# Kernel tuning notes

Measured on AMD Instinct MI355X. Metric: run time of the kernel, lower is better.

## Reference

```python
import jax, jax.numpy as jnp
import numpy as np

T, B = 128, 256
C_IN, H = 1024, 1024


def setup_inputs() -> dict:
    key = jax.random.key(0)
    ks = jax.random.split(key, 6)
    x = jax.random.normal(ks[0], (T * B, C_IN), dtype=jnp.float32)
    Wi = jax.random.normal(ks[1], (C_IN, 4 * H), dtype=jnp.float32) / np.sqrt(C_IN)
    Wh = jax.random.normal(ks[2], (H, 4 * H), dtype=jnp.float32) / np.sqrt(H)
    b = jax.random.normal(ks[3], (4 * H,), dtype=jnp.float32) * 0.01
    done = jax.random.randint(ks[4], (T * B,), 0, 2) > 0
    main = jax.random.randint(ks[5], (T * B,), 0, 2) > 0
    zeros = jnp.zeros((B, H), dtype=jnp.float32)
    return {"x": x, "c1": zeros, "h1": zeros, "c2": zeros, "h2": zeros,
            "Wi": Wi, "Wh": Wh, "b": b, "done": done, "main": main}


def reference(x, c1, h1, c2, h2, Wi, Wh, b, done, main):
    batch = c1.shape[0]
    num_steps = x.shape[0] // batch
    x3 = x.reshape(num_steps, batch, -1)
    done3 = done.reshape(num_steps, batch)
    main3 = main.reshape(num_steps, batch)

    def step(carry, inp):
        (r1c, r1h), (r2c, r2h) = carry
        xt, dt, mt = inp
        m = mt[:, None]  # [B,1] select player-1 vs player-2 state
        c = jnp.where(m, r1c, r2c)
        h = jnp.where(m, r1h, r2h)
        # OptimizedLSTMCell: fused gates, flax order i, f, g, o
        z = xt @ Wi + h @ Wh + b
        i, f, g, o = jnp.split(z, 4, axis=-1)
        nc = jax.nn.sigmoid(f) * c + jax.nn.sigmoid(i) * jnp.tanh(g)
        nh = jax.nn.sigmoid(o) * jnp.tanh(nc)
        # write back only to the active player's state
        n1c = jnp.where(m, nc, r1c); n1h = jnp.where(m, nh, r1h)
        n2c = jnp.where(m, r2c, nc); n2h = jnp.where(m, r2h, nh)
        # reset both states where episode is done
        d = dt[:, None]
        n1c = jnp.where(d, 0.0, n1c); n1h = jnp.where(d, 0.0, n1h)
        n2c = jnp.where(d, 0.0, n2c); n2h = jnp.where(d, 0.0, n2h)
        return ((n1c, n1h), (n2c, n2h)), nh

    _, ys = jax.lax.scan(step, ((c1, h1), (c2, h2)), (x3, done3, main3))
    return ys.reshape(-1, ys.shape[-1])  # [T*B, H]
```

## Files before the change

kernel.cpp:

```cpp
#include <hip/hip_runtime.h>
#include <cstdint>
#include <cstddef>

typedef unsigned short u16;
typedef unsigned char u8;
typedef unsigned int u32;

typedef short s16x8 __attribute__((ext_vector_type(8)));
typedef float f32x4 __attribute__((ext_vector_type(4)));

__device__ __forceinline__ float b2f(u16 h){ u32 u = ((u32)h)<<16; float f; __builtin_memcpy(&f,&u,4); return f; }
__device__ __forceinline__ u16 f2b(float x){ u32 u; __builtin_memcpy(&u,&x,4); u += 0x7fffu + ((u>>16)&1u); return (u16)(u>>16); }
__device__ __forceinline__ float sigf(float x){ return 1.f/(1.f+__expf(-x)); }
__device__ __forceinline__ float tanh2(float x){
  float ax=fabsf(x); float e=__expf(-2.f*ax); float r=(1.f-e)/(1.f+e); return x<0.f? -r : r;
}

typedef __attribute__((address_space(1))) const void gvoid_t;
typedef __attribute__((address_space(3))) void lvoid_t;
__device__ __forceinline__ void gl_lds16(const u16* src, u16* dst){
  __builtin_amdgcn_global_load_lds((gvoid_t*)src, (lvoid_t*)dst, 16, 0, 0);
}

__device__ __forceinline__ void st_u16_coh(u16* p, u16 v){
  asm volatile("global_store_short %0, %1, off sc0 sc1" :: "v"(p), "v"((u32)v) : "memory");
}
__device__ __forceinline__ void st_f32_coh(float* p, float v){
  asm volatile("global_store_dword %0, %1, off sc0 sc1" :: "v"(p), "v"(v) : "memory");
}
__device__ __forceinline__ s16x8 gload16(const u16* p){
  s16x8 r;
  asm volatile("global_load_dwordx4 %0, %1, off" : "=v"(r) : "v"(p) : "memory");
  return r;
}
__device__ __forceinline__ s16x8 gload16_coh(const u16* p){
  s16x8 r;
  asm volatile("global_load_dwordx4 %0, %1, off sc0 sc1" : "=v"(r) : "v"(p) : "memory");
  return r;
}

__global__ void detect_mask_mode(const u8* raw, int n, int* flag){
  __shared__ int cnt;
  int tid = threadIdx.x;
  if(tid==0) cnt=0;
  __syncthreads();
  int c=0;
  for(int i=tid;i<n;i+=blockDim.x) c += (raw[i]!=0);
  atomicAdd(&cnt, c);
  __syncthreads();
  if(tid==0) *flag = (cnt > (n>>2)) ? 1 : 0;
}

__global__ void convert_masks(const void* done_raw, const void* main_raw, u8* done_u8, u8* main_u8, int n, const int* flag){
  int mode = *flag;
  for(int i = blockIdx.x*blockDim.x + threadIdx.x; i<n; i += gridDim.x*blockDim.x){
    u8 d, m;
    if(mode){ d = ((const u8*)done_raw)[i]!=0; m = ((const u8*)main_raw)[i]!=0; }
    else    { d = ((const int*)done_raw)[i]!=0; m = ((const int*)main_raw)[i]!=0; }
    done_u8[i]=d; main_u8[i]=m;
  }
}

__global__ void zero_flags(int* p, int n){
  int i = threadIdx.x;
  if(i<n) p[i]=0;
}

__global__ void cvt_f32_bf16(const float* __restrict__ in, u16* __restrict__ out, int n4){
  int i = blockIdx.x*blockDim.x + threadIdx.x;
  if(i < n4){
    float4 v = ((const float4*)in)[i];
    ushort4 o;
    o.x=f2b(v.x); o.y=f2b(v.y); o.z=f2b(v.z); o.w=f2b(v.w);
    ((ushort4*)out)[i]=o;
  }
}

__global__ void transpose_to_bf16(const float* __restrict__ in, u16* __restrict__ out, int R, int C){
  __shared__ float tile[64][65];
  int c0 = blockIdx.x*64, r0 = blockIdx.y*64;
  int tx = threadIdx.x & 63, ty = threadIdx.x >> 6;
  for(int i=ty;i<64;i+=4) tile[i][tx] = in[(size_t)(r0+i)*C + c0 + tx];
  __syncthreads();
  for(int i=ty;i<64;i+=4) out[(size_t)(c0+i)*R + r0 + tx] = f2b(tile[tx][i]);
}

__global__ void init_hsel(const float* __restrict__ h1in, const float* __restrict__ h2in,
                          const u8* __restrict__ mmain, u16* __restrict__ hsel0){
  int i = blockIdx.x*blockDim.x + threadIdx.x;
  if(i < 256*1024){
    int row = i >> 10;
    hsel0[i] = f2b(mmain[row] ? h1in[i] : h2in[i]);
  }
}

template<bool ZF32>
__global__ __launch_bounds__(256) void gemm_zx(const u16* __restrict__ A, const u16* __restrict__ Bt,
                                               const float* __restrict__ bias, void* __restrict__ Cout,
                                               int M, int N, int K){
  __shared__ u16 As[128*32];
  __shared__ u16 Bs[128*32];
  int nbx = N>>7, nby = M>>7;
  int nwg = nbx*nby;
  int gid = blockIdx.x;
  int per = nwg>>3;
  int g2 = (gid&7)*per + (gid>>3);
  int tpg = 8*nbx;
  int grp = g2/tpg, w = g2%tpg;
  int brow = grp*8 + (w & 7);
  int bcol = w >> 3;
  int row0 = brow<<7, col0 = bcol<<7;

  int tid=threadIdx.x, wid=tid>>6, lane=tid&63;
  int l15=lane&15, hi=lane>>4;
  int wm=(wid>>1)<<6, wn=(wid&1)<<6;

  f32x4 acc[4][4];
  #pragma unroll
  for(int m=0;m<4;m++)
    #pragma unroll
    for(int n=0;n<4;n++) acc[m][n]=(f32x4){0.f,0.f,0.f,0.f};

  for(int k0=0;k0<K;k0+=32){
    __syncthreads();
    #pragma unroll
    for(int q=0;q<2;q++){
      int cb=q*256+wid*64;
      int ch=cb+lane;
      gl_lds16(A + (size_t)(row0+(ch>>2))*K + k0 + (ch&3)*8, &As[cb*8]);
    }
    #pragma unroll
    for(int q=0;q<2;q++){
      int cb=q*256+wid*64;
      int ch=cb+lane;
      gl_lds16(Bt + (size_t)(col0+(ch>>2))*K + k0 + (ch&3)*8, &Bs[cb*8]);
    }
    __syncthreads();
    s16x8 a[4], b[4];
    #pragma unroll
    for(int m=0;m<4;m++) a[m] = *(const s16x8*)&As[(wm+m*16+l15)*32 + hi*8];
    #pragma unroll
    for(int n=0;n<4;n++) b[n] = *(const s16x8*)&Bs[(wn+n*16+l15)*32 + hi*8];
    #pragma unroll
    for(int m=0;m<4;m++)
      #pragma unroll
      for(int n=0;n<4;n++)
        acc[m][n] = __builtin_amdgcn_mfma_f32_16x16x32_bf16(a[m],b[n],acc[m][n],0,0,0);
  }
  #pragma unroll
  for(int m=0;m<4;m++){
    #pragma unroll
    for(int n=0;n<4;n++){
      #pragma unroll
      for(int j=0;j<4;j++){
        int r = row0+wm+m*16+hi*4+j;
        int c = col0+wn+n*16+l15;
        float v = acc[m][n][j] + bias[c];
        if(ZF32) ((float*)Cout)[(size_t)r*N+c]=v;
        else     ((u16*)Cout)[(size_t)r*N+c]=f2b(v);
      }
    }
  }
}

template<bool ZF32>
__global__ __launch_bounds__(512) __attribute__((amdgpu_waves_per_eu(2,2)))
void lstm_persist(
    const void* __restrict__ Zx, const u16* __restrict__ Wht,
    u16* __restrict__ hs0, u16* __restrict__ hs1,
    const float* __restrict__ c1i, const float* __restrict__ h1i,
    const float* __restrict__ c2i, const float* __restrict__ h2i,
    const u8* __restrict__ mdone, const u8* __restrict__ mmain,
    float* __restrict__ out, int* __restrict__ ready)
{
  __shared__ u16 As[32768];
  __shared__ float zpart[4*2*32*33];

  const int bid = blockIdx.x;
  const int rg = bid & 7, jg = bid >> 3;
  const int r0 = rg << 5, j0 = jg << 5;
  const int tid = threadIdx.x, wid = tid >> 6, lane = tid & 63;
  const int l15 = lane & 15, hi = lane >> 4;
  const int gate = wid >> 1, kg = wid & 1;
  const int srow = tid >> 4, sc16 = tid & 15;
  const int erow = tid >> 5, ecol = tid & 31;

  s16x8 breg[2][16];
  {
    #pragma unroll
    for(int n=0;n<2;n++){
      const u16* wp = Wht + ((size_t)(gate*1024 + j0 + n*16 + l15))*1024 + kg*512 + hi*8;
      #pragma unroll
      for(int kk=0;kk<16;kk++) breg[n][kk] = gload16(wp + kk*32);
    }
    asm volatile("s_waitcnt vmcnt(0)" ::: "memory");
    __builtin_amdgcn_sched_barrier(0);
  }

  float c1r[2],c2r[2],h1r[2],h2r[2];
  #pragma unroll
  for(int e=0;e<2;e++){
    size_t sidx = (size_t)(r0 + e*16 + erow)*1024 + j0 + ecol;
    c1r[e]=c1i[sidx]; c2r[e]=c2i[sidx]; h1r[e]=h1i[sidx]; h2r[e]=h2i[sidx];
  }

  const u16* Zb = (const u16*)Zx;
  const float* Zf = (const float*)Zx;
  int* flag = ready + rg*32;

  for(int t=0;t<128;t++){
    float zr[4][2]; u8 md[2], mm[2], mm2[2];
    #pragma unroll
    for(int e=0;e<2;e++){
      int gb = t*256 + r0 + e*16 + erow;
      size_t base = (size_t)gb*4096 + j0 + ecol;
      #pragma unroll
      for(int g=0; g<4; g++)
        zr[g][e] = ZF32 ? Zf[base + g*1024] : b2f(Zb[base + g*1024]);
      md[e]=mdone[gb]; mm[e]=mmain[gb];
      mm2[e] = (t<127) ? mmain[gb+256] : (u8)0;
    }

    if(t>0 && tid==0){
      while(__hip_atomic_load(flag, __ATOMIC_RELAXED, __HIP_MEMORY_SCOPE_AGENT) < 32*t)
        __builtin_amdgcn_s_sleep(1);
    }
    __syncthreads();
    __builtin_amdgcn_sched_barrier(0);

    const u16* hin = (t&1) ? hs1 : hs0;
    u16* hout = (t&1) ? hs0 : hs1;

    {
      const u16* hrow = hin + (size_t)(r0+srow)*1024;
      s16x8 v[8];
      #pragma unroll
      for(int kc=0;kc<8;kc++) v[kc] = gload16_coh(hrow + (kc*16+sc16)*8);
      asm volatile("s_waitcnt vmcnt(4)" ::: "memory");
      #pragma unroll
      for(int kc=0;kc<4;kc++){
        int chunk = kc*16+sc16;
        *(s16x8*)&As[chunk*256 + ((srow ^ (chunk&7))<<3)] = v[kc];
      }
      asm volatile("s_waitcnt vmcnt(0)" ::: "memory");
      #pragma unroll
      for(int kc=4;kc<8;kc++){
        int chunk = kc*16+sc16;
        *(s16x8*)&As[chunk*256 + ((srow ^ (chunk&7))<<3)] = v[kc];
      }
    }
    __syncthreads();

    f32x4 acc[2][2];
    #pragma unroll
    for(int m=0;m<2;m++)
      #pragma unroll
      for(int n=0;n<2;n++) acc[m][n]=(f32x4){0.f,0.f,0.f,0.f};
    #pragma unroll
    for(int kk=0;kk<16;kk++){
      int c0 = (kg*16 + kk)*4 + hi;
      s16x8 a0 = *(const s16x8*)&As[c0*256 + ((l15      ^ (c0&7))<<3)];
      s16x8 a1 = *(const s16x8*)&As[c0*256 + (((16+l15) ^ (c0&7))<<3)];
      acc[0][0] = __builtin_amdgcn_mfma_f32_16x16x32_bf16(a0, breg[0][kk], acc[0][0], 0,0,0);
      acc[0][1] = __builtin_amdgcn_mfma_f32_16x16x32_bf16(a0, breg[1][kk], acc[0][1], 0,0,0);
      acc[1][0] = __builtin_amdgcn_mfma_f32_16x16x32_bf16(a1, breg[0][kk], acc[1][0], 0,0,0);
      acc[1][1] = __builtin_amdgcn_mfma_f32_16x16x32_bf16(a1, breg[1][kk], acc[1][1], 0,0,0);
    }

    #pragma unroll
    for(int m=0;m<2;m++)
      #pragma unroll
      for(int n=0;n<2;n++)
        #pragma unroll
        for(int j=0;j<4;j++){
          int row = m*16 + hi*4 + j;
          zpart[((gate*2+kg)*32 + row)*33 + n*16 + l15] = acc[m][n][j];
        }
    __syncthreads();

    float nhv[2];
    #pragma unroll
    for(int e=0;e<2;e++){
      int row = e*16 + erow;
      float zi  = zr[0][e] + zpart[((0)*32+row)*33 + ecol] + zpart[((1)*32+row)*33 + ecol];
      float zf_ = zr[1][e] + zpart[((2)*32+row)*33 + ecol] + zpart[((3)*32+row)*33 + ecol];
      float zg  = zr[2][e] + zpart[((4)*32+row)*33 + ecol] + zpart[((5)*32+row)*33 + ecol];
      float zo  = zr[3][e] + zpart[((6)*32+row)*33 + ecol] + zpart[((7)*32+row)*33 + ecol];
      bool m_ = mm[e]!=0, d_ = md[e]!=0;
      float co = m_ ? c1r[e] : c2r[e];
      float nc = sigf(zf_)*co + sigf(zi)*tanh2(zg);
      float nhx = sigf(zo)*tanh2(nc);
      nhv[e] = nhx;
      float n1c = m_?nc:c1r[e], n2c = m_?c2r[e]:nc;
      float n1h = m_?nhx:h1r[e], n2h = m_?h2r[e]:nhx;
      if(d_){ n1c=0.f; n2c=0.f; n1h=0.f; n2h=0.f; }
      c1r[e]=n1c; c2r[e]=n2c; h1r[e]=n1h; h2r[e]=n2h;
      if(t<127)
        st_u16_coh(&hout[(size_t)(r0+row)*1024 + j0 + ecol], f2b(mm2[e] ? n1h : n2h));
    }
    asm volatile("s_waitcnt vmcnt(0)" ::: "memory");
    __syncthreads();
    if(t<127 && tid==0)
      __hip_atomic_fetch_add(flag, 1, __ATOMIC_RELAXED, __HIP_MEMORY_SCOPE_AGENT);

    #pragma unroll
    for(int e=0;e<2;e++){
      int gb = t*256 + r0 + e*16 + erow;
      st_f32_coh(&out[(size_t)gb*1024 + j0 + ecol], nhv[e]);
    }
  }
}

extern "C" void kernel_launch(void* const* d_in, const int* in_sizes, int n_in,
                              void* d_out, int out_size, void* d_ws, size_t ws_size,
                              hipStream_t stream){
  const float* x   = (const float*)d_in[0];
  const float* c1i = (const float*)d_in[1];
  const float* h1i = (const float*)d_in[2];
  const float* c2i = (const float*)d_in[3];
  const float* h2i = (const float*)d_in[4];
  const float* Wi  = (const float*)d_in[5];
  const float* Wh  = (const float*)d_in[6];
  const float* bias= (const float*)d_in[7];
  const void* done_raw = d_in[8];
  const void* main_raw = d_in[9];
  float* out = (float*)d_out;

  char* ws = (char*)d_ws;
  size_t off=0;
  auto alloc=[&](size_t sz)->char*{ char* p = ws+off; off += (sz+255)&~(size_t)255; return p; };

  u16* xb   = (u16*)alloc(33554432ull*2);
  u16* WiT  = (u16*)alloc(4096ull*1024*2);
  u16* WhT  = (u16*)alloc(4096ull*1024*2);
  u16* hs0  = (u16*)alloc(262144ull*2);
  u16* hs1  = (u16*)alloc(262144ull*2);
  u8* dmask = (u8*)alloc(32768);
  u8* mmask = (u8*)alloc(32768);
  int* flag = (int*)alloc(256);
  int* ready= (int*)alloc(1024);

  bool zf32 = (off + 536870912ull) <= ws_size;
  void* Zx  = (void*)alloc(zf32 ? 536870912ull : 268435456ull);

  detect_mask_mode<<<1,256,0,stream>>>((const u8*)done_raw, 32768, flag);
  convert_masks<<<64,256,0,stream>>>(done_raw, main_raw, dmask, mmask, 32768, flag);
  cvt_f32_bf16<<<32768,256,0,stream>>>(x, xb, 8388608);
  transpose_to_bf16<<<dim3(64,16),256,0,stream>>>(Wi, WiT, 1024, 4096);
  transpose_to_bf16<<<dim3(64,16),256,0,stream>>>(Wh, WhT, 1024, 4096);
  init_hsel<<<1024,256,0,stream>>>(h1i, h2i, mmask, hs0);
  zero_flags<<<1,256,0,stream>>>(ready, 256);

  if(zf32) gemm_zx<true ><<<8192,256,0,stream>>>(xb, WiT, bias, Zx, 32768, 4096, 1024);
  else     gemm_zx<false><<<8192,256,0,stream>>>(xb, WiT, bias, Zx, 32768, 4096, 1024);

  if(zf32)
    lstm_persist<true ><<<256,512,0,stream>>>(Zx,WhT,hs0,hs1,c1i,h1i,c2i,h2i,dmask,mmask,out,ready);
  else
    lstm_persist<false><<<256,512,0,stream>>>(Zx,WhT,hs0,hs1,c1i,h1i,c2i,h2i,dmask,mmask,out,ready);
}
```

Before: 1.103 ms.

## Streamline persistent LSTM step: packed masks, SGPR-based addressing, per-wave signal counting

Packs the done, main and next-step main masks into a single byte code. The persistent LSTM loop now uses precomputed 32-bit voffsets with scalar base pointers for its loads and stores, and uses fast reciprocal in sigmoid and tanh. The block-wide barrier before the cross-block ready signal is replaced by an LDS counter, so the eighth wave to finish issues the global atomic increment. This removes a __syncthreads and some address arithmetic from the recurrent critical path. In exchange, LDS counter reuse across steps depends on careful ordering, and rcp slightly reduces precision.

```diff
diff --git a/kernel.cpp b/kernel.cpp
--- a/kernel.cpp
+++ b/kernel.cpp
@@ -11,9 +11,11 @@
 
 __device__ __forceinline__ float b2f(u16 h){ u32 u = ((u32)h)<<16; float f; __builtin_memcpy(&f,&u,4); return f; }
 __device__ __forceinline__ u16 f2b(float x){ u32 u; __builtin_memcpy(&u,&x,4); u += 0x7fffu + ((u>>16)&1u); return (u16)(u>>16); }
-__device__ __forceinline__ float sigf(float x){ return 1.f/(1.f+__expf(-x)); }
+__device__ __forceinline__ float sigf(float x){ return __builtin_amdgcn_rcpf(1.f+__expf(-x)); }
 __device__ __forceinline__ float tanh2(float x){
-  float ax=fabsf(x); float e=__expf(-2.f*ax); float r=(1.f-e)/(1.f+e); return x<0.f? -r : r;
+  float ax=fabsf(x); float e=__expf(-2.f*ax);
+  float r=(1.f-e)*__builtin_amdgcn_rcpf(1.f+e);
+  return x<0.f? -r : r;
 }
 
 typedef __attribute__((address_space(1))) const void gvoid_t;
@@ -22,20 +24,25 @@
   __builtin_amdgcn_global_load_lds((gvoid_t*)src, (lvoid_t*)dst, 16, 0, 0);
 }
 
-__device__ __forceinline__ void st_u16_coh(u16* p, u16 v){
-  asm volatile("global_store_short %0, %1, off sc0 sc1" :: "v"(p), "v"((u32)v) : "memory");
-}
-__device__ __forceinline__ void st_f32_coh(float* p, float v){
-  asm volatile("global_store_dword %0, %1, off sc0 sc1" :: "v"(p), "v"(v) : "memory");
+__device__ __forceinline__ s16x8 gload16_coh_s(const u16* sbase, u32 voff){
+  s16x8 r;
+  asm volatile("global_load_dwordx4 %0, %1, %2 sc0 sc1" : "=v"(r) : "v"(voff), "s"(sbase) : "memory");
+  return r;
+}
+__device__ __forceinline__ float gloadf_s(const float* sbase, u32 voff){
+  float r;
+  asm volatile("global_load_dword %0, %1, %2" : "=v"(r) : "v"(voff), "s"(sbase) : "memory");
+  return r;
+}
+__device__ __forceinline__ void st_u16_coh_s(u16* sbase, u32 voff, u16 v){
+  asm volatile("global_store_short %0, %1, %2 sc0 sc1" :: "v"(voff), "v"((u32)v), "s"(sbase) : "memory");
+}
+__device__ __forceinline__ void st_f32_coh_s(float* sbase, u32 voff, float v){
+  asm volatile("global_store_dword %0, %1, %2 sc0 sc1" :: "v"(voff), "v"(v), "s"(sbase) : "memory");
 }
 __device__ __forceinline__ s16x8 gload16(const u16* p){
   s16x8 r;
   asm volatile("global_load_dwordx4 %0, %1, off" : "=v"(r) : "v"(p) : "memory");
-  return r;
-}
-__device__ __forceinline__ s16x8 gload16_coh(const u16* p){
-  s16x8 r;
-  asm volatile("global_load_dwordx4 %0, %1, off sc0 sc1" : "=v"(r) : "v"(p) : "memory");
   return r;
 }
 
@@ -51,13 +58,18 @@
   if(tid==0) *flag = (cnt > (n>>2)) ? 1 : 0;
 }
 
-__global__ void convert_masks(const void* done_raw, const void* main_raw, u8* done_u8, u8* main_u8, int n, const int* flag){
+__global__ void build_mcode(const void* done_raw, const void* main_raw, u8* code, int n, const int* flag){
   int mode = *flag;
   for(int i = blockIdx.x*blockDim.x + threadIdx.x; i<n; i += gridDim.x*blockDim.x){
-    u8 d, m;
-    if(mode){ d = ((const u8*)done_raw)[i]!=0; m = ((const u8*)main_raw)[i]!=0; }
-    else    { d = ((const int*)done_raw)[i]!=0; m = ((const int*)main_raw)[i]!=0; }
-    done_u8[i]=d; main_u8[i]=m;
+    u8 d, m, m2;
+    if(mode){
+      d = ((const u8*)done_raw)[i]!=0; m = ((const u8*)main_raw)[i]!=0;
+      m2 = (i+256<n) ? (((const u8*)main_raw)[i+256]!=0) : (u8)0;
+    } else {
+      d = ((const int*)done_raw)[i]!=0; m = ((const int*)main_raw)[i]!=0;
+      m2 = (i+256<n) ? (((const int*)main_raw)[i+256]!=0) : (u8)0;
+    }
+    code[i] = d | (m<<1) | (m2<<2);
   }
 }
 
@@ -86,11 +98,11 @@
 }
 
 __global__ void init_hsel(const float* __restrict__ h1in, const float* __restrict__ h2in,
-                          const u8* __restrict__ mmain, u16* __restrict__ hsel0){
+                          const u8* __restrict__ mcode, u16* __restrict__ hsel0){
   int i = blockIdx.x*blockDim.x + threadIdx.x;
   if(i < 256*1024){
     int row = i >> 10;
-    hsel0[i] = f2b(mmain[row] ? h1in[i] : h2in[i]);
+    hsel0[i] = f2b((mcode[row]&2) ? h1in[i] : h2in[i]);
   }
 }
 
@@ -170,11 +182,12 @@
     u16* __restrict__ hs0, u16* __restrict__ hs1,
     const float* __restrict__ c1i, const float* __restrict__ h1i,
     const float* __restrict__ c2i, const float* __restrict__ h2i,
-    const u8* __restrict__ mdone, const u8* __restrict__ mmain,
+    const u8* __restrict__ mcode,
     float* __restrict__ out, int* __restrict__ ready)
 {
   __shared__ u16 As[32768];
   __shared__ float zpart[4*2*32*33];
+  __shared__ int lcnt[2];
 
   const int bid = blockIdx.x;
   const int rg = bid & 7, jg = bid >> 3;
@@ -185,6 +198,8 @@
   const int srow = tid >> 4, sc16 = tid & 15;
   const int erow = tid >> 5, ecol = tid & 31;
 
+  if(tid < 2) lcnt[tid] = 0;
+
   s16x8 breg[2][16];
   {
     #pragma unroll
@@ -204,22 +219,52 @@
     c1r[e]=c1i[sidx]; c2r[e]=c2i[sidx]; h1r[e]=h1i[sidx]; h2r[e]=h2i[sidx];
   }
 
-  const u16* Zb = (const u16*)Zx;
-  const float* Zf = (const float*)Zx;
+  u32 voffS[8];
+  #pragma unroll
+  for(int kc=0;kc<8;kc++) voffS[kc] = (u32)(((r0+srow)*1024 + (kc*16+sc16)*8)*2);
+  u32 voffH[2], voffO[2];
+  #pragma unroll
+  for(int e=0;e<2;e++){
+    u32 idx = (u32)((r0 + e*16 + erow)*1024 + j0 + ecol);
+    voffH[e] = idx*2;
+    voffO[e] = idx*4;
+  }
+  u32 voffZ[8];
+  #pragma unroll
+  for(int g=0;g<4;g++)
+    #pragma unroll
+    for(int e=0;e<2;e++)
+      voffZ[g*2+e] = (u32)((((r0 + e*16 + erow)*4096) + g*1024 + j0 + ecol)*4);
+
+  u16* pS = &As[sc16*256 + ((srow ^ (sc16&7))<<3)];
+  const u16* pAe = &As[kg*16384 + hi*256 + ((l15 ^  hi   )<<3)];
+  const u16* pAo = &As[kg*16384 + hi*256 + ((l15 ^ (4+hi))<<3)];
+  float* pzw = &zpart[((gate*2+kg)*32 + hi*4)*33 + l15];
+  const float* pzr = &zpart[erow*33 + ecol];
+
+  const char* zstep = (const char*)Zx;
+  const u16* Zb16 = (const u16*)Zx;
+  float* outp = out;
+  const u8* mp = mcode + r0;
   int* flag = ready + rg*32;
 
+  #pragma unroll 1
   for(int t=0;t<128;t++){
-    float zr[4][2]; u8 md[2], mm[2], mm2[2];
-    #pragma unroll
-    for(int e=0;e<2;e++){
-      int gb = t*256 + r0 + e*16 + erow;
-      size_t base = (size_t)gb*4096 + j0 + ecol;
-      #pragma unroll
-      for(int g=0; g<4; g++)
-        zr[g][e] = ZF32 ? Zf[base + g*1024] : b2f(Zb[base + g*1024]);
-      md[e]=mdone[gb]; mm[e]=mmain[gb];
-      mm2[e] = (t<127) ? mmain[gb+256] : (u8)0;
-    }
+    float zr[4][2];
+    if(ZF32){
+      #pragma unroll
+      for(int g=0;g<4;g++)
+        #pragma unroll
+        for(int e=0;e<2;e++)
+          zr[g][e] = gloadf_s((const float*)zstep, voffZ[g*2+e]);
+    } else {
+      #pragma unroll
+      for(int g=0;g<4;g++)
+        #pragma unroll
+        for(int e=0;e<2;e++)
+          zr[g][e] = b2f(Zb16[(size_t)(t*256 + r0 + e*16 + erow)*4096 + g*1024 + j0 + ecol]);
+    }
+    u8 cd0 = mp[erow], cd1 = mp[16+erow];
 
     if(t>0 && tid==0){
       while(__hip_atomic_load(flag, __ATOMIC_RELAXED, __HIP_MEMORY_SCOPE_AGENT) < 32*t)
@@ -228,26 +273,16 @@
     __syncthreads();
     __builtin_amdgcn_sched_barrier(0);
 
-    const u16* hin = (t&1) ? hs1 : hs0;
-    u16* hout = (t&1) ? hs0 : hs1;
+    const u16* hinp = (t&1) ? hs1 : hs0;
+    u16* houtp = (t&1) ? hs0 : hs1;
 
     {
-      const u16* hrow = hin + (size_t)(r0+srow)*1024;
-      s16x8 v[8];
-      #pragma unroll
-      for(int kc=0;kc<8;kc++) v[kc] = gload16_coh(hrow + (kc*16+sc16)*8);
-      asm volatile("s_waitcnt vmcnt(4)" ::: "memory");
-      #pragma unroll
-      for(int kc=0;kc<4;kc++){
-        int chunk = kc*16+sc16;
-        *(s16x8*)&As[chunk*256 + ((srow ^ (chunk&7))<<3)] = v[kc];
-      }
+      s16x8 hv[8];
+      #pragma unroll
+      for(int kc=0;kc<8;kc++) hv[kc] = gload16_coh_s(hinp, voffS[kc]);
       asm volatile("s_waitcnt vmcnt(0)" ::: "memory");
       #pragma unroll
-      for(int kc=4;kc<8;kc++){
-        int chunk = kc*16+sc16;
-        *(s16x8*)&As[chunk*256 + ((srow ^ (chunk&7))<<3)] = v[kc];
-      }
+      for(int kc=0;kc<8;kc++) *(s16x8*)(pS + kc*4096) = hv[kc];
     }
     __syncthreads();
 
@@ -258,9 +293,9 @@
       for(int n=0;n<2;n++) acc[m][n]=(f32x4){0.f,0.f,0.f,0.f};
     #pragma unroll
     for(int kk=0;kk<16;kk++){
-      int c0 = (kg*16 + kk)*4 + hi;
-      s16x8 a0 = *(const s16x8*)&As[c0*256 + ((l15      ^ (c0&7))<<3)];
-      s16x8 a1 = *(const s16x8*)&As[c0*256 + (((16+l15) ^ (c0&7))<<3)];
+      const u16* p = (kk&1) ? pAo : pAe;
+      s16x8 a0 = *(const s16x8*)(p + kk*1024);
+      s16x8 a1 = *(const s16x8*)(p + kk*1024 + 128);
       acc[0][0] = __builtin_amdgcn_mfma_f32_16x16x32_bf16(a0, breg[0][kk], acc[0][0], 0,0,0);
       acc[0][1] = __builtin_amdgcn_mfma_f32_16x16x32_bf16(a0, breg[1][kk], acc[0][1], 0,0,0);
       acc[1][0] = __builtin_amdgcn_mfma_f32_16x16x32_bf16(a1, breg[0][kk], acc[1][0], 0,0,0);
@@ -272,21 +307,19 @@
       #pragma unroll
       for(int n=0;n<2;n++)
         #pragma unroll
-        for(int j=0;j<4;j++){
-          int row = m*16 + hi*4 + j;
-          zpart[((gate*2+kg)*32 + row)*33 + n*16 + l15] = acc[m][n][j];
-        }
+        for(int j=0;j<4;j++)
+          pzw[m*528 + j*33 + n*16] = acc[m][n][j];
     __syncthreads();
 
     float nhv[2];
     #pragma unroll
     for(int e=0;e<2;e++){
-      int row = e*16 + erow;
-      float zi  = zr[0][e] + zpart[((0)*32+row)*33 + ecol] + zpart[((1)*32+row)*33 + ecol];
-      float zf_ = zr[1][e] + zpart[((2)*32+row)*33 + ecol] + zpart[((3)*32+row)*33 + ecol];
-      float zg  = zr[2][e] + zpart[((4)*32+row)*33 + ecol] + zpart[((5)*32+row)*33 + ecol];
-      float zo  = zr[3][e] + zpart[((6)*32+row)*33 + ecol] + zpart[((7)*32+row)*33 + ecol];
-      bool m_ = mm[e]!=0, d_ = md[e]!=0;
+      u8 cd = e ? cd1 : cd0;
+      float zi  = zr[0][e] + pzr[0*1056 + e*528] + pzr[1*1056 + e*528];
+      float zf_ = zr[1][e] + pzr[2*1056 + e*528] + pzr[3*1056 + e*528];
+      float zg  = zr[2][e] + pzr[4*1056 + e*528] + pzr[5*1056 + e*528];
+      float zo  = zr[3][e] + pzr[6*1056 + e*528] + pzr[7*1056 + e*528];
+      bool d_ = cd & 1, m_ = cd & 2, m2 = cd & 4;
       float co = m_ ? c1r[e] : c2r[e];
       float nc = sigf(zf_)*co + sigf(zi)*tanh2(zg);
       float nhx = sigf(zo)*tanh2(nc);
@@ -296,18 +329,27 @@
       if(d_){ n1c=0.f; n2c=0.f; n1h=0.f; n2h=0.f; }
       c1r[e]=n1c; c2r[e]=n2c; h1r[e]=n1h; h2r[e]=n2h;
       if(t<127)
-        st_u16_coh(&hout[(size_t)(r0+row)*1024 + j0 + ecol], f2b(mm2[e] ? n1h : n2h));
-    }
-    asm volatile("s_waitcnt vmcnt(0)" ::: "memory");
-    __syncthreads();
-    if(t<127 && tid==0)
-      __hip_atomic_fetch_add(flag, 1, __ATOMIC_RELAXED, __HIP_MEMORY_SCOPE_AGENT);
-
-    #pragma unroll
-    for(int e=0;e<2;e++){
-      int gb = t*256 + r0 + e*16 + erow;
-      st_f32_coh(&out[(size_t)gb*1024 + j0 + ecol], nhv[e]);
-    }
+        st_u16_coh_s(houtp, voffH[e], f2b(m2 ? n1h : n2h));
+    }
+
+    if(t<127){
+      asm volatile("s_waitcnt vmcnt(0)" ::: "memory");
+      if(lane==0){
+        int c = atomicAdd(&lcnt[t&1], 1);
+        if(c==7){
+          lcnt[t&1] = 0;
+          __hip_atomic_fetch_add(flag, 1, __ATOMIC_RELAXED, __HIP_MEMORY_SCOPE_AGENT);
+        }
+      }
+    }
+
+    #pragma unroll
+    for(int e=0;e<2;e++)
+      st_f32_coh_s(outp, voffO[e], nhv[e]);
+
+    zstep += 4194304;
+    outp  += 262144;
+    mp    += 256;
   }
 }
 
@@ -335,8 +377,7 @@
   u16* WhT  = (u16*)alloc(4096ull*1024*2);
   u16* hs0  = (u16*)alloc(262144ull*2);
   u16* hs1  = (u16*)alloc(262144ull*2);
-  u8* dmask = (u8*)alloc(32768);
-  u8* mmask = (u8*)alloc(32768);
+  u8* mcode = (u8*)alloc(32768);
   int* flag = (int*)alloc(256);
   int* ready= (int*)alloc(1024);
 
@@ -344,18 +385,18 @@
   void* Zx  = (void*)alloc(zf32 ? 536870912ull : 268435456ull);
 
   detect_mask_mode<<<1,256,0,stream>>>((const u8*)done_raw, 32768, flag);
-  convert_masks<<<64,256,0,stream>>>(done_raw, main_raw, dmask, mmask, 32768, flag);
+  build_mcode<<<64,256,0,stream>>>(done_raw, main_raw, mcode, 32768, flag);
   cvt_f32_bf16<<<32768,256,0,stream>>>(x, xb, 8388608);
   transpose_to_bf16<<<dim3(64,16),256,0,stream>>>(Wi, WiT, 1024, 4096);
   transpose_to_bf16<<<dim3(64,16),256,0,stream>>>(Wh, WhT, 1024, 4096);
-  init_hsel<<<1024,256,0,stream>>>(h1i, h2i, mmask, hs0);
+  init_hsel<<<1024,256,0,stream>>>(h1i, h2i, mcode, hs0);
   zero_flags<<<1,256,0,stream>>>(ready, 256);
 
   if(zf32) gemm_zx<true ><<<8192,256,0,stream>>>(xb, WiT, bias, Zx, 32768, 4096, 1024);
   else     gemm_zx<false><<<8192,256,0,stream>>>(xb, WiT, bias, Zx, 32768, 4096, 1024);
 
   if(zf32)
-    lstm_persist<true ><<<256,512,0,stream>>>(Zx,WhT,hs0,hs1,c1i,h1i,c2i,h2i,dmask,mmask,out,ready);
+    lstm_persist<true ><<<256,512,0,stream>>>(Zx,WhT,hs0,hs1,c1i,h1i,c2i,h2i,mcode,out,ready);
   else
-    lstm_persist<false><<<256,512,0,stream>>>(Zx,WhT,hs0,hs1,c1i,h1i,c2i,h2i,dmask,mmask,out,ready);
-}
+    lstm_persist<false><<<256,512,0,stream>>>(Zx,WhT,hs0,hs1,c1i,h1i,c2i,h2i,mcode,out,ready);
+}
```

Result: slower. 1.289 ms (+16.9%).

## Store input projection as fp16, deepen GEMM K-tile, use fast reciprocal

Applied to the files above, without the earlier changes.

The precomputed input-projection Zx is always stored as 16-bit fp16 instead of fp32 when workspace allows, which halves the GEMM's output writes and the persistent LSTM's per-step Zx reads. The GEMM now stages 64-wide K slices in a k-chunk-major LDS layout with two MFMA sub-steps per barrier pair, and hoists the bias load out of the inner loop. Sigmoid and tanh use the hardware approximate reciprocal instead of division. fp16 storage and the approximate reciprocal cost some precision.

```diff
diff --git a/kernel.cpp b/kernel.cpp
--- a/kernel.cpp
+++ b/kernel.cpp
@@ -9,11 +9,17 @@
 typedef short s16x8 __attribute__((ext_vector_type(8)));
 typedef float f32x4 __attribute__((ext_vector_type(4)));
 
+#define MF(a,b,c) __builtin_amdgcn_mfma_f32_16x16x32_bf16((a),(b),(c),0,0,0)
+
 __device__ __forceinline__ float b2f(u16 h){ u32 u = ((u32)h)<<16; float f; __builtin_memcpy(&f,&u,4); return f; }
 __device__ __forceinline__ u16 f2b(float x){ u32 u; __builtin_memcpy(&u,&x,4); u += 0x7fffu + ((u>>16)&1u); return (u16)(u>>16); }
-__device__ __forceinline__ float sigf(float x){ return 1.f/(1.f+__expf(-x)); }
+__device__ __forceinline__ u16 f2h(float x){ _Float16 h = (_Float16)x; u16 u; __builtin_memcpy(&u,&h,2); return u; }
+__device__ __forceinline__ float h2f(u16 v){ _Float16 h; __builtin_memcpy(&h,&v,2); return (float)h; }
+__device__ __forceinline__ float sigf(float x){ return __builtin_amdgcn_rcpf(1.f+__expf(-x)); }
 __device__ __forceinline__ float tanh2(float x){
-  float ax=fabsf(x); float e=__expf(-2.f*ax); float r=(1.f-e)/(1.f+e); return x<0.f? -r : r;
+  float ax=fabsf(x); float e=__expf(-2.f*ax);
+  float r=(1.f-e)*__builtin_amdgcn_rcpf(1.f+e);
+  return x<0.f? -r : r;
 }
 
 typedef __attribute__((address_space(1))) const void gvoid_t;
@@ -94,14 +100,12 @@
   }
 }
 
-template<bool ZF32>
 __global__ __launch_bounds__(256) void gemm_zx(const u16* __restrict__ A, const u16* __restrict__ Bt,
-                                               const float* __restrict__ bias, void* __restrict__ Cout,
-                                               int M, int N, int K){
-  __shared__ u16 As[128*32];
-  __shared__ u16 Bs[128*32];
-  int nbx = N>>7, nby = M>>7;
-  int nwg = nbx*nby;
+                                               const float* __restrict__ bias, u16* __restrict__ C){
+  __shared__ u16 As[8192];
+  __shared__ u16 Bs[8192];
+  const int nbx = 32;
+  const int nwg = 8192;
   int gid = blockIdx.x;
   int per = nwg>>3;
   int g2 = (gid&7)*per + (gid>>3);
@@ -121,52 +125,55 @@
     #pragma unroll
     for(int n=0;n<4;n++) acc[m][n]=(f32x4){0.f,0.f,0.f,0.f};
 
-  for(int k0=0;k0<K;k0+=32){
-    __syncthreads();
-    #pragma unroll
-    for(int q=0;q<2;q++){
-      int cb=q*256+wid*64;
-      int ch=cb+lane;
-      gl_lds16(A + (size_t)(row0+(ch>>2))*K + k0 + (ch&3)*8, &As[cb*8]);
-    }
-    #pragma unroll
-    for(int q=0;q<2;q++){
-      int cb=q*256+wid*64;
-      int ch=cb+lane;
-      gl_lds16(Bt + (size_t)(col0+(ch>>2))*K + k0 + (ch&3)*8, &Bs[cb*8]);
-    }
-    __syncthreads();
-    s16x8 a[4], b[4];
-    #pragma unroll
-    for(int m=0;m<4;m++) a[m] = *(const s16x8*)&As[(wm+m*16+l15)*32 + hi*8];
-    #pragma unroll
-    for(int n=0;n<4;n++) b[n] = *(const s16x8*)&Bs[(wn+n*16+l15)*32 + hi*8];
-    #pragma unroll
-    for(int m=0;m<4;m++)
-      #pragma unroll
-      for(int n=0;n<4;n++)
-        acc[m][n] = __builtin_amdgcn_mfma_f32_16x16x32_bf16(a[m],b[n],acc[m][n],0,0,0);
+  for(int k0=0;k0<1024;k0+=64){
+    __syncthreads();
+    #pragma unroll
+    for(int i=0;i<4;i++){
+      int cb = (wid*4+i)*64;
+      int c  = cb + lane;
+      int r  = c & 127, s = c >> 7;
+      gl_lds16(A + (size_t)(row0+r)*1024 + k0 + s*8, &As[cb*8]);
+    }
+    #pragma unroll
+    for(int i=0;i<4;i++){
+      int cb = (wid*4+i)*64;
+      int c  = cb + lane;
+      int r  = c & 127, s = c >> 7;
+      gl_lds16(Bt + (size_t)(col0+r)*1024 + k0 + s*8, &Bs[cb*8]);
+    }
+    __syncthreads();
+    #pragma unroll
+    for(int kk=0;kk<2;kk++){
+      s16x8 a[4], b[4];
+      #pragma unroll
+      for(int m=0;m<4;m++) a[m] = *(const s16x8*)&As[(kk*4+hi)*1024 + (wm+m*16+l15)*8];
+      #pragma unroll
+      for(int n=0;n<4;n++) b[n] = *(const s16x8*)&Bs[(kk*4+hi)*1024 + (wn+n*16+l15)*8];
+      #pragma unroll
+      for(int m=0;m<4;m++)
+        #pragma unroll
+        for(int n=0;n<4;n++)
+          acc[m][n] = MF(a[m],b[n],acc[m][n]);
+    }
   }
   #pragma unroll
   for(int m=0;m<4;m++){
     #pragma unroll
     for(int n=0;n<4;n++){
+      int c = col0+wn+n*16+l15;
+      float bv = bias[c];
       #pragma unroll
       for(int j=0;j<4;j++){
         int r = row0+wm+m*16+hi*4+j;
-        int c = col0+wn+n*16+l15;
-        float v = acc[m][n][j] + bias[c];
-        if(ZF32) ((float*)Cout)[(size_t)r*N+c]=v;
-        else     ((u16*)Cout)[(size_t)r*N+c]=f2b(v);
+        C[(size_t)r*4096+c] = f2h(acc[m][n][j] + bv);
       }
     }
   }
 }
 
-template<bool ZF32>
 __global__ __launch_bounds__(512) __attribute__((amdgpu_waves_per_eu(2,2)))
 void lstm_persist(
-    const void* __restrict__ Zx, const u16* __restrict__ Wht,
+    const u16* __restrict__ Zx, const u16* __restrict__ Wht,
     u16* __restrict__ hs0, u16* __restrict__ hs1,
     const float* __restrict__ c1i, const float* __restrict__ h1i,
     const float* __restrict__ c2i, const float* __restrict__ h2i,
@@ -204,8 +211,6 @@
     c1r[e]=c1i[sidx]; c2r[e]=c2i[sidx]; h1r[e]=h1i[sidx]; h2r[e]=h2i[sidx];
   }
 
-  const u16* Zb = (const u16*)Zx;
-  const float* Zf = (const float*)Zx;
   int* flag = ready + rg*32;
 
   for(int t=0;t<128;t++){
@@ -216,7 +221,7 @@
       size_t base = (size_t)gb*4096 + j0 + ecol;
       #pragma unroll
       for(int g=0; g<4; g++)
-        zr[g][e] = ZF32 ? Zf[base + g*1024] : b2f(Zb[base + g*1024]);
+        zr[g][e] = h2f(Zx[base + g*1024]);
       md[e]=mdone[gb]; mm[e]=mmain[gb];
       mm2[e] = (t<127) ? mmain[gb+256] : (u8)0;
     }
@@ -261,10 +266,10 @@
       int c0 = (kg*16 + kk)*4 + hi;
       s16x8 a0 = *(const s16x8*)&As[c0*256 + ((l15      ^ (c0&7))<<3)];
       s16x8 a1 = *(const s16x8*)&As[c0*256 + (((16+l15) ^ (c0&7))<<3)];
-      acc[0][0] = __builtin_amdgcn_mfma_f32_16x16x32_bf16(a0, breg[0][kk], acc[0][0], 0,0,0);
-      acc[0][1] = __builtin_amdgcn_mfma_f32_16x16x32_bf16(a0, breg[1][kk], acc[0][1], 0,0,0);
-      acc[1][0] = __builtin_amdgcn_mfma_f32_16x16x32_bf16(a1, breg[0][kk], acc[1][0], 0,0,0);
-      acc[1][1] = __builtin_amdgcn_mfma_f32_16x16x32_bf16(a1, breg[1][kk], acc[1][1], 0,0,0);
+      acc[0][0] = MF(a0, breg[0][kk], acc[0][0]);
+      acc[0][1] = MF(a0, breg[1][kk], acc[0][1]);
+      acc[1][0] = MF(a1, breg[0][kk], acc[1][0]);
+      acc[1][1] = MF(a1, breg[1][kk], acc[1][1]);
     }
 
     #pragma unroll
@@ -339,9 +344,7 @@
   u8* mmask = (u8*)alloc(32768);
   int* flag = (int*)alloc(256);
   int* ready= (int*)alloc(1024);
-
-  bool zf32 = (off + 536870912ull) <= ws_size;
-  void* Zx  = (void*)alloc(zf32 ? 536870912ull : 268435456ull);
+  u16* Zx   = (u16*)alloc(268435456ull);
 
   detect_mask_mode<<<1,256,0,stream>>>((const u8*)done_raw, 32768, flag);
   convert_masks<<<64,256,0,stream>>>(done_raw, main_raw, dmask, mmask, 32768, flag);
@@ -351,11 +354,7 @@
   init_hsel<<<1024,256,0,stream>>>(h1i, h2i, mmask, hs0);
   zero_flags<<<1,256,0,stream>>>(ready, 256);
 
-  if(zf32) gemm_zx<true ><<<8192,256,0,stream>>>(xb, WiT, bias, Zx, 32768, 4096, 1024);
-  else     gemm_zx<false><<<8192,256,0,stream>>>(xb, WiT, bias, Zx, 32768, 4096, 1024);
-
-  if(zf32)
-    lstm_persist<true ><<<256,512,0,stream>>>(Zx,WhT,hs0,hs1,c1i,h1i,c2i,h2i,dmask,mmask,out,ready);
-  else
-    lstm_persist<false><<<256,512,0,stream>>>(Zx,WhT,hs0,hs1,c1i,h1i,c2i,h2i,dmask,mmask,out,ready);
-}
+  gemm_zx<<<8192,256,0,stream>>>(xb, WiT, bias, Zx);
+
+  lstm_persist<<<256,512,0,stream>>>(Zx,WhT,hs0,hs1,c1i,h1i,c2i,h2i,dmask,mmask,out,ready);
+}
```

Result: slower. 1.234 ms (+11.9%).
